# Performance work log

Measured on AMD Instinct MI355X. Metric: run time of the kernel, lower is better.

Reference implementation:

```python
import jax, jax.numpy as jnp
import numpy as np

ALPHA = 1.702  # sigmoid-GLU scale
LIMIT = 7.0    # clamp limit
TOP_K = 2      # num_experts_per_tok


def setup_inputs() -> dict:
    key = jax.random.key(0)
    ks = jax.random.split(key, 4)
    B, S, H, E, I = 2, 1024, 1024, 8, 2048
    return {
        "hidden_states": jax.random.normal(ks[0], (B, S, H), jnp.float32),
        "router_weight": jax.random.normal(ks[1], (E, H), jnp.float32),
        "router_bias": jnp.zeros((E,), jnp.float32),
        "gate_up_proj": jax.random.normal(ks[2], (E, H, 2 * I), jnp.float32) * 0.02,
        "gate_up_bias": jnp.zeros((E, 2 * I), jnp.float32),
        "down_proj": jax.random.normal(ks[3], (E, I, H), jnp.float32) * 0.02,
        "down_bias": jnp.zeros((E, H), jnp.float32),
    }


def reference(hidden_states, router_weight, router_bias, gate_up_proj,
              gate_up_bias, down_proj, down_bias):
    B, S, H = hidden_states.shape
    E, _, two_I = gate_up_proj.shape
    I = two_I // 2

    flat = hidden_states.reshape(B * S, H)  # [T, H]

    # Router: softmax + top-k
    logits = flat @ router_weight.T + router_bias            # [T, E]
    scores = jax.nn.softmax(logits, axis=-1)
    topk_w, topk_idx = jax.lax.top_k(scores, TOP_K)          # [T, K]

    # Dense per-expert gated FFN (einsum 'abmh,ehn->abemn' computes all experts
    # on all tokens; the reshape/permute dance is a mathematical no-op).
    gu = jnp.einsum('th,ehn->ten', flat, gate_up_proj) + gate_up_bias  # [T, E, 2I]
    gate = jnp.minimum(gu[..., :I], LIMIT)
    up = jnp.clip(gu[..., I:], -LIMIT, LIMIT)
    glu = gate * jax.nn.sigmoid(gate * ALPHA)
    act = (up + 1.0) * glu                                   # [T, E, I]

    down = jnp.einsum('tei,eih->teh', act, down_proj) + down_bias  # [T, E, H]

    # Combine: gather each token's top-k expert outputs, weighted sum.
    gathered = jnp.take_along_axis(down, topk_idx[:, :, None], axis=1)  # [T, K, H]
    out = (gathered * topk_w[:, :, None]).sum(axis=1)        # [T, H]
    return out.reshape(B, S, H)
```

## Files before the change

### kernel.cpp

```cpp
#include <hip/hip_runtime.h>
#include <math.h>

#define TT 2048
#define HH 1024
#define EE 8
#define II 2048
#define N1 4096
#define ALPHA 1.702f
#define LIMIT 7.0f

typedef __attribute__((ext_vector_type(8))) short short8;
typedef __attribute__((ext_vector_type(4))) float floatx4;

__device__ __forceinline__ short f2bf(float f) {
  union { float f; unsigned u; } v; v.f = f;
  unsigned r = (v.u + 0x7fffu + ((v.u >> 16) & 1u)) >> 16;
  return (short)r;
}
__device__ __forceinline__ float bf2f(unsigned short s) {
  union { unsigned u; float f; } v; v.u = ((unsigned)s) << 16;
  return v.f;
}

__global__ __launch_bounds__(256) void router_kernel(
    const float* __restrict__ x, const float* __restrict__ rw,
    const float* __restrict__ rb, int* __restrict__ topk_idx,
    float* __restrict__ topk_w) {
  const int t = blockIdx.x;
  const float* xr = x + (size_t)t * HH;
  const int lane = threadIdx.x & 63;
  const int wave = threadIdx.x >> 6;
  float xv[16];
#pragma unroll
  for (int i = 0; i < 16; i++) xv[i] = xr[lane + i * 64];
  __shared__ float logits[EE];
#pragma unroll
  for (int ee = 0; ee < 2; ee++) {
    const int e = wave * 2 + ee;
    const float* wr = rw + (size_t)e * HH;
    float s = 0.f;
#pragma unroll
    for (int i = 0; i < 16; i++) s += xv[i] * wr[lane + i * 64];
#pragma unroll
    for (int off = 32; off > 0; off >>= 1) s += __shfl_down(s, off, 64);
    if (lane == 0) logits[e] = s + rb[e];
  }
  __syncthreads();
  if (threadIdx.x == 0) {
    float l[EE], sc[EE];
    float mx = -3.4e38f;
    for (int i = 0; i < EE; i++) { l[i] = logits[i]; mx = fmaxf(mx, l[i]); }
    float sum = 0.f;
    for (int i = 0; i < EE; i++) { sc[i] = expf(l[i] - mx); sum += sc[i]; }
    const float inv = 1.f / sum;
    int i0 = 0;
    for (int i = 1; i < EE; i++) if (sc[i] > sc[i0]) i0 = i;
    int i1 = (i0 == 0) ? 1 : 0;
    for (int i = 0; i < EE; i++) if (i != i0 && sc[i] > sc[i1]) i1 = i;
    topk_idx[t * 2 + 0] = i0;
    topk_idx[t * 2 + 1] = i1;
    topk_w[t * 2 + 0] = sc[i0] * inv;
    topk_w[t * 2 + 1] = sc[i1] * inv;
  }
}

__global__ void assign_kernel(const int* __restrict__ topk_idx,
                              int* __restrict__ counts, int* __restrict__ rows) {
  const int id = blockIdx.x * blockDim.x + threadIdx.x;
  if (id >= TT * 2) return;
  const int e = topk_idx[id];
  const int slot = atomicAdd(&counts[e], 1);
  rows[e * TT + slot] = id;
}

__global__ __launch_bounds__(256) void gemm_gu(
    const float* __restrict__ x, const float* __restrict__ gup,
    const float* __restrict__ gub, const int* __restrict__ counts,
    const int* __restrict__ rows, unsigned short* __restrict__ gu) {
  const int e = blockIdx.z, mtile = blockIdx.y, ntile = blockIdx.x;
  const int count = counts[e];
  if (mtile * 128 >= count) return;
  const int* rl = rows + e * TT + mtile * 128;
  __shared__ short As[128][40];
  __shared__ short Bs[128][40];
  const int tid = threadIdx.x;
  const int lane = tid & 63, wave = tid >> 6;
  const int wm = (wave & 1) << 6, wn = (wave >> 1) << 6;
  const int quad = lane >> 4, r16 = lane & 15;

  const int arow = tid >> 2, akoct = tid & 3;
  const int cr0 = (mtile * 128 + arow < count) ? arow : (count - 1 - mtile * 128);
  const int cr1 = (mtile * 128 + arow + 64 < count) ? arow + 64 : (count - 1 - mtile * 128);
  const float* a0 = x + (size_t)(rl[cr0] >> 1) * HH;
  const float* a1 = x + (size_t)(rl[cr1] >> 1) * HH;

  const int bn = tid & 127, bk = tid >> 7;
  const float* bb = gup + (size_t)e * HH * N1 + ntile * 128 + bn;

  floatx4 acc[4][4] = {};

  for (int k0 = 0; k0 < HH; k0 += 32) {
    __syncthreads();
    {
      const float4* p = (const float4*)(a0 + k0 + akoct * 8);
      float4 v0 = p[0], v1 = p[1];
      short8 s;
      s[0]=f2bf(v0.x); s[1]=f2bf(v0.y); s[2]=f2bf(v0.z); s[3]=f2bf(v0.w);
      s[4]=f2bf(v1.x); s[5]=f2bf(v1.y); s[6]=f2bf(v1.z); s[7]=f2bf(v1.w);
      *(short8*)&As[arow][akoct * 8] = s;
      p = (const float4*)(a1 + k0 + akoct * 8);
      v0 = p[0]; v1 = p[1];
      s[0]=f2bf(v0.x); s[1]=f2bf(v0.y); s[2]=f2bf(v0.z); s[3]=f2bf(v0.w);
      s[4]=f2bf(v1.x); s[5]=f2bf(v1.y); s[6]=f2bf(v1.z); s[7]=f2bf(v1.w);
      *(short8*)&As[arow + 64][akoct * 8] = s;
    }
    {
      const float* p = bb + (size_t)(k0 + bk * 8) * N1;
      short8 s;
#pragma unroll
      for (int j = 0; j < 8; j++) s[j] = f2bf(p[(size_t)j * N1]);
      *(short8*)&Bs[bn][bk * 8] = s;
      p = bb + (size_t)(k0 + (bk + 2) * 8) * N1;
#pragma unroll
      for (int j = 0; j < 8; j++) s[j] = f2bf(p[(size_t)j * N1]);
      *(short8*)&Bs[bn][(bk + 2) * 8] = s;
    }
    __syncthreads();
    short8 af[4], bf_[4];
#pragma unroll
    for (int i = 0; i < 4; i++)
      af[i] = *(const short8*)&As[wm + i * 16 + r16][quad * 8];
#pragma unroll
    for (int j = 0; j < 4; j++)
      bf_[j] = *(const short8*)&Bs[wn + j * 16 + r16][quad * 8];
#pragma unroll
    for (int i = 0; i < 4; i++)
#pragma unroll
      for (int j = 0; j < 4; j++)
        acc[i][j] = __builtin_amdgcn_mfma_f32_16x16x32_bf16(af[i], bf_[j], acc[i][j], 0, 0, 0);
  }
#pragma unroll
  for (int i = 0; i < 4; i++) {
#pragma unroll
    for (int reg = 0; reg < 4; reg++) {
      const int rrow = wm + i * 16 + quad * 4 + reg;
      if (mtile * 128 + rrow < count) {
        const int ent = rl[rrow];
        unsigned short* orow = gu + (size_t)ent * N1 + ntile * 128;
#pragma unroll
        for (int j = 0; j < 4; j++) {
          const int c = wn + j * 16 + r16;
          const float v = acc[i][j][reg] + gub[e * N1 + ntile * 128 + c];
          orow[c] = (unsigned short)f2bf(v);
        }
      }
    }
  }
}

__global__ void act_kernel(const unsigned short* __restrict__ gu,
                           unsigned short* __restrict__ act) {
  const int id = blockIdx.x * blockDim.x + threadIdx.x;
  if (id >= TT * 2 * II) return;
  const int r = id >> 11;
  const int i = id & (II - 1);
  float g = bf2f(gu[(size_t)r * N1 + i]);
  float u = bf2f(gu[(size_t)r * N1 + II + i]);
  g = fminf(g, LIMIT);
  u = fminf(fmaxf(u, -LIMIT), LIMIT);
  const float glu = g / (1.f + expf(-g * ALPHA));
  act[(size_t)r * II + i] = (unsigned short)f2bf((u + 1.f) * glu);
}

__global__ __launch_bounds__(256) void gemm_down(
    const unsigned short* __restrict__ act, const float* __restrict__ dp,
    const float* __restrict__ db, const int* __restrict__ counts,
    const int* __restrict__ rows, float* __restrict__ dout) {
  const int e = blockIdx.z, mtile = blockIdx.y, ntile = blockIdx.x;
  const int count = counts[e];
  if (mtile * 128 >= count) return;
  const int* rl = rows + e * TT + mtile * 128;
  __shared__ short As[128][40];
  __shared__ short Bs[128][40];
  const int tid = threadIdx.x;
  const int lane = tid & 63, wave = tid >> 6;
  const int wm = (wave & 1) << 6, wn = (wave >> 1) << 6;
  const int quad = lane >> 4, r16 = lane & 15;

  const int arow = tid >> 2, akoct = tid & 3;
  const int cr0 = (mtile * 128 + arow < count) ? arow : (count - 1 - mtile * 128);
  const int cr1 = (mtile * 128 + arow + 64 < count) ? arow + 64 : (count - 1 - mtile * 128);
  const unsigned short* a0 = act + (size_t)rl[cr0] * II;
  const unsigned short* a1 = act + (size_t)rl[cr1] * II;

  const int bn = tid & 127, bk = tid >> 7;
  const float* bb = dp + (size_t)e * II * HH + ntile * 128 + bn;

  floatx4 acc[4][4] = {};

  for (int k0 = 0; k0 < II; k0 += 32) {
    __syncthreads();
    {
      *(short8*)&As[arow][akoct * 8] = *(const short8*)(a0 + k0 + akoct * 8);
      *(short8*)&As[arow + 64][akoct * 8] = *(const short8*)(a1 + k0 + akoct * 8);
    }
    {
      const float* p = bb + (size_t)(k0 + bk * 8) * HH;
      short8 s;
#pragma unroll
      for (int j = 0; j < 8; j++) s[j] = f2bf(p[(size_t)j * HH]);
      *(short8*)&Bs[bn][bk * 8] = s;
      p = bb + (size_t)(k0 + (bk + 2) * 8) * HH;
#pragma unroll
      for (int j = 0; j < 8; j++) s[j] = f2bf(p[(size_t)j * HH]);
      *(short8*)&Bs[bn][(bk + 2) * 8] = s;
    }
    __syncthreads();
    short8 af[4], bf_[4];
#pragma unroll
    for (int i = 0; i < 4; i++)
      af[i] = *(const short8*)&As[wm + i * 16 + r16][quad * 8];
#pragma unroll
    for (int j = 0; j < 4; j++)
      bf_[j] = *(const short8*)&Bs[wn + j * 16 + r16][quad * 8];
#pragma unroll
    for (int i = 0; i < 4; i++)
#pragma unroll
      for (int j = 0; j < 4; j++)
        acc[i][j] = __builtin_amdgcn_mfma_f32_16x16x32_bf16(af[i], bf_[j], acc[i][j], 0, 0, 0);
  }
#pragma unroll
  for (int i = 0; i < 4; i++) {
#pragma unroll
    for (int reg = 0; reg < 4; reg++) {
      const int rrow = wm + i * 16 + quad * 4 + reg;
      if (mtile * 128 + rrow < count) {
        const int ent = rl[rrow];
        float* orow = dout + (size_t)ent * HH + ntile * 128;
#pragma unroll
        for (int j = 0; j < 4; j++) {
          const int c = wn + j * 16 + r16;
          orow[c] = acc[i][j][reg] + db[e * HH + ntile * 128 + c];
        }
      }
    }
  }
}

__global__ void combine_kernel(const float* __restrict__ dout,
                               const float* __restrict__ tw,
                               float* __restrict__ out) {
  const int id = blockIdx.x * blockDim.x + threadIdx.x;
  const int t = id >> 8;
  const int h = (id & 255) * 4;
  const float w0 = tw[t * 2], w1 = tw[t * 2 + 1];
  const float4 a = *(const float4*)(dout + (size_t)(2 * t) * HH + h);
  const float4 b = *(const float4*)(dout + (size_t)(2 * t + 1) * HH + h);
  float4 o;
  o.x = w0 * a.x + w1 * b.x;
  o.y = w0 * a.y + w1 * b.y;
  o.z = w0 * a.z + w1 * b.z;
  o.w = w0 * a.w + w1 * b.w;
  *(float4*)(out + (size_t)t * HH + h) = o;
}

extern "C" void kernel_launch(void* const* d_in, const int* in_sizes, int n_in,
                              void* d_out, int out_size, void* d_ws, size_t ws_size,
                              hipStream_t stream) {
  const float* x   = (const float*)d_in[0];
  const float* rw  = (const float*)d_in[1];
  const float* rb  = (const float*)d_in[2];
  const float* gup = (const float*)d_in[3];
  const float* gub = (const float*)d_in[4];
  const float* dp  = (const float*)d_in[5];
  const float* db  = (const float*)d_in[6];
  float* out = (float*)d_out;

  char* ws = (char*)d_ws;
  int*   topk_idx = (int*)(ws + 0);
  float* topk_w   = (float*)(ws + 16384);
  int*   counts   = (int*)(ws + 32768);
  int*   rows     = (int*)(ws + 33024);
  unsigned short* gu  = (unsigned short*)(ws + 131072);
  unsigned short* act = (unsigned short*)(ws + 131072 + 33554432);
  float* dout = (float*)(ws + 131072 + 33554432 + 16777216);

  router_kernel<<<TT, 256, 0, stream>>>(x, rw, rb, topk_idx, topk_w);
  hipMemsetAsync(counts, 0, 64, stream);
  assign_kernel<<<(TT * 2 + 255) / 256, 256, 0, stream>>>(topk_idx, counts, rows);
  gemm_gu<<<dim3(N1 / 128, TT / 128, EE), 256, 0, stream>>>(x, gup, gub, counts, rows, gu);
  act_kernel<<<(TT * 2 * II) / 256, 256, 0, stream>>>(gu, act);
  gemm_down<<<dim3(HH / 128, TT / 128, EE), 256, 0, stream>>>(act, dp, db, counts, rows, dout);
  combine_kernel<<<(TT * HH / 4) / 256, 256, 0, stream>>>(dout, topk_w, out);
}
```

Before: 452.9 us.

## Pre-convert weights to transposed bf16, use global_load_lds, compact schedule, split-K down

Adds pre-pass kernels that convert x to bf16 and transpose/convert both expert weight tensors to K-contiguous bf16 on every call. Both GEMMs can then stage tiles with direct global-to-LDS 16-byte loads into a swizzled layout, replacing the strided scalar fp32 loads and in-loop conversion. A compact schedule of (expert, m-tile) pairs replaces the mostly-empty 3D grid. The down GEMM is split in two along K with atomic accumulation into a zeroed buffer, and its bias moves into combine. The activation kernel is vectorized. The transposes add a full read and write of roughly 200 MB of fp32 weights per call, and the atomics add contention.

```diff
diff --git a/kernel.cpp b/kernel.cpp
--- a/kernel.cpp
+++ b/kernel.cpp
@@ -8,9 +8,15 @@
 #define N1 4096
 #define ALPHA 1.702f
 #define LIMIT 7.0f
+#define MAXSCHED 40
+#define SPLITK 2
 
 typedef __attribute__((ext_vector_type(8))) short short8;
 typedef __attribute__((ext_vector_type(4))) float floatx4;
+
+#define GLL(g, l) __builtin_amdgcn_global_load_lds(                          \
+    (const __attribute__((address_space(1))) void*)(g),                      \
+    (__attribute__((address_space(3))) void*)(l), 16, 0, 0)
 
 __device__ __forceinline__ short f2bf(float f) {
   union { float f; unsigned u; } v; v.f = f;
@@ -20,6 +26,48 @@
 __device__ __forceinline__ float bf2f(unsigned short s) {
   union { unsigned u; float f; } v; v.u = ((unsigned)s) << 16;
   return v.f;
+}
+
+__global__ __launch_bounds__(256) void convert_x(const float* __restrict__ x,
+                                                 unsigned short* __restrict__ xb) {
+  const size_t off = ((size_t)blockIdx.x * blockDim.x + threadIdx.x) * 8;
+  const float4 v0 = *(const float4*)(x + off);
+  const float4 v1 = *(const float4*)(x + off + 4);
+  short8 s;
+  s[0]=f2bf(v0.x); s[1]=f2bf(v0.y); s[2]=f2bf(v0.z); s[3]=f2bf(v0.w);
+  s[4]=f2bf(v1.x); s[5]=f2bf(v1.y); s[6]=f2bf(v1.z); s[7]=f2bf(v1.w);
+  *(short8*)(xb + off) = s;
+}
+
+__global__ __launch_bounds__(256) void transpose_cvt(const float* __restrict__ src,
+                                                     unsigned short* __restrict__ dst,
+                                                     int K, int N) {
+  const int e = blockIdx.z;
+  src += (size_t)e * K * N;
+  dst += (size_t)e * K * N;
+  const int k0 = blockIdx.y * 64, n0 = blockIdx.x * 64;
+  __shared__ unsigned short Ts[64][66];
+  const int tid = threadIdx.x;
+  const int c4 = (tid & 15) * 4;
+  const int r = tid >> 4;
+#pragma unroll
+  for (int i = 0; i < 4; i++) {
+    const int kk = r + i * 16;
+    const float4 v = *(const float4*)(src + (size_t)(k0 + kk) * N + n0 + c4);
+    Ts[kk][c4 + 0] = (unsigned short)f2bf(v.x);
+    Ts[kk][c4 + 1] = (unsigned short)f2bf(v.y);
+    Ts[kk][c4 + 2] = (unsigned short)f2bf(v.z);
+    Ts[kk][c4 + 3] = (unsigned short)f2bf(v.w);
+  }
+  __syncthreads();
+#pragma unroll
+  for (int i = 0; i < 4; i++) {
+    const int nn = r + i * 16;
+    unsigned short o[4];
+#pragma unroll
+    for (int j = 0; j < 4; j++) o[j] = Ts[c4 + j][nn];
+    *(uint2*)(dst + (size_t)(n0 + nn) * K + k0 + c4) = *(const uint2*)o;
+  }
 }
 
 __global__ __launch_bounds__(256) void router_kernel(
@@ -47,11 +95,11 @@
   }
   __syncthreads();
   if (threadIdx.x == 0) {
-    float l[EE], sc[EE];
+    float sc[EE];
     float mx = -3.4e38f;
-    for (int i = 0; i < EE; i++) { l[i] = logits[i]; mx = fmaxf(mx, l[i]); }
+    for (int i = 0; i < EE; i++) mx = fmaxf(mx, logits[i]);
     float sum = 0.f;
-    for (int i = 0; i < EE; i++) { sc[i] = expf(l[i] - mx); sum += sc[i]; }
+    for (int i = 0; i < EE; i++) { sc[i] = expf(logits[i] - mx); sum += sc[i]; }
     const float inv = 1.f / sum;
     int i0 = 0;
     for (int i = 1; i < EE; i++) if (sc[i] > sc[i0]) i0 = i;
@@ -73,194 +121,225 @@
   rows[e * TT + slot] = id;
 }
 
+__global__ void sched_kernel(const int* __restrict__ counts,
+                             int* __restrict__ sched, int* __restrict__ nsched) {
+  if (threadIdx.x == 0) {
+    int n = 0;
+    for (int e = 0; e < EE; e++) {
+      const int mt = (counts[e] + 127) >> 7;
+      for (int m = 0; m < mt; m++) sched[n++] = (e << 8) | m;
+    }
+    nsched[0] = n;
+  }
+}
+
 __global__ __launch_bounds__(256) void gemm_gu(
-    const float* __restrict__ x, const float* __restrict__ gup,
-    const float* __restrict__ gub, const int* __restrict__ counts,
-    const int* __restrict__ rows, unsigned short* __restrict__ gu) {
-  const int e = blockIdx.z, mtile = blockIdx.y, ntile = blockIdx.x;
-  const int count = counts[e];
-  if (mtile * 128 >= count) return;
+    const unsigned short* __restrict__ x_bf,
+    const unsigned short* __restrict__ gup_t,
+    const float* __restrict__ gub,
+    const int* __restrict__ counts, const int* __restrict__ rows,
+    const int* __restrict__ sched, const int* __restrict__ nsched,
+    unsigned short* __restrict__ gu) {
+  const int sid = blockIdx.y;
+  if (sid >= nsched[0]) return;
+  const int sv = sched[sid];
+  const int e = sv >> 8, mtile = sv & 255;
+  const int count = counts[e] - mtile * 128;
+  const int ntile = blockIdx.x;
   const int* rl = rows + e * TT + mtile * 128;
-  __shared__ short As[128][40];
-  __shared__ short Bs[128][40];
+
+  __shared__ short As[128 * 32];
+  __shared__ short Bs[128 * 32];
+
   const int tid = threadIdx.x;
   const int lane = tid & 63, wave = tid >> 6;
+  const int quad = lane >> 4, r16 = lane & 15;
   const int wm = (wave & 1) << 6, wn = (wave >> 1) << 6;
-  const int quad = lane >> 4, r16 = lane & 15;
-
-  const int arow = tid >> 2, akoct = tid & 3;
-  const int cr0 = (mtile * 128 + arow < count) ? arow : (count - 1 - mtile * 128);
-  const int cr1 = (mtile * 128 + arow + 64 < count) ? arow + 64 : (count - 1 - mtile * 128);
-  const float* a0 = x + (size_t)(rl[cr0] >> 1) * HH;
-  const float* a1 = x + (size_t)(rl[cr1] >> 1) * HH;
-
-  const int bn = tid & 127, bk = tid >> 7;
-  const float* bb = gup + (size_t)e * HH * N1 + ntile * 128 + bn;
+
+  const int srow = lane >> 2;
+  const int soct = (lane & 3) ^ (srow & 3);
+  const int lr0 = wave * 32 + srow;
+  const int lr1 = lr0 + 16;
+  const int cr0 = (lr0 < count) ? lr0 : 0;
+  const int cr1 = (lr1 < count) ? lr1 : 0;
+  const unsigned short* aptr0 = x_bf + (size_t)(rl[cr0] >> 1) * HH + soct * 8;
+  const unsigned short* aptr1 = x_bf + (size_t)(rl[cr1] >> 1) * HH + soct * 8;
+  const unsigned short* bptr0 = gup_t + (size_t)e * N1 * HH +
+                                (size_t)(ntile * 128 + lr0) * HH + soct * 8;
+  const unsigned short* bptr1 = bptr0 + (size_t)16 * HH;
+
+  short* lA0 = As + (wave * 32) * 32;
+  short* lA1 = As + (wave * 32 + 16) * 32;
+  short* lB0 = Bs + (wave * 32) * 32;
+  short* lB1 = Bs + (wave * 32 + 16) * 32;
+
+  const int fcol = (quad ^ (r16 & 3)) * 8;
+  const short8* ap[4]; const short8* bp[4];
+#pragma unroll
+  for (int i = 0; i < 4; i++) {
+    ap[i] = (const short8*)&As[(wm + i * 16 + r16) * 32 + fcol];
+    bp[i] = (const short8*)&Bs[(wn + i * 16 + r16) * 32 + fcol];
+  }
 
   floatx4 acc[4][4] = {};
-
   for (int k0 = 0; k0 < HH; k0 += 32) {
     __syncthreads();
-    {
-      const float4* p = (const float4*)(a0 + k0 + akoct * 8);
-      float4 v0 = p[0], v1 = p[1];
-      short8 s;
-      s[0]=f2bf(v0.x); s[1]=f2bf(v0.y); s[2]=f2bf(v0.z); s[3]=f2bf(v0.w);
-      s[4]=f2bf(v1.x); s[5]=f2bf(v1.y); s[6]=f2bf(v1.z); s[7]=f2bf(v1.w);
-      *(short8*)&As[arow][akoct * 8] = s;
-      p = (const float4*)(a1 + k0 + akoct * 8);
-      v0 = p[0]; v1 = p[1];
-      s[0]=f2bf(v0.x); s[1]=f2bf(v0.y); s[2]=f2bf(v0.z); s[3]=f2bf(v0.w);
-      s[4]=f2bf(v1.x); s[5]=f2bf(v1.y); s[6]=f2bf(v1.z); s[7]=f2bf(v1.w);
-      *(short8*)&As[arow + 64][akoct * 8] = s;
-    }
-    {
-      const float* p = bb + (size_t)(k0 + bk * 8) * N1;
-      short8 s;
-#pragma unroll
-      for (int j = 0; j < 8; j++) s[j] = f2bf(p[(size_t)j * N1]);
-      *(short8*)&Bs[bn][bk * 8] = s;
-      p = bb + (size_t)(k0 + (bk + 2) * 8) * N1;
-#pragma unroll
-      for (int j = 0; j < 8; j++) s[j] = f2bf(p[(size_t)j * N1]);
-      *(short8*)&Bs[bn][(bk + 2) * 8] = s;
-    }
+    GLL(aptr0 + k0, lA0);
+    GLL(aptr1 + k0, lA1);
+    GLL(bptr0 + k0, lB0);
+    GLL(bptr1 + k0, lB1);
     __syncthreads();
     short8 af[4], bf_[4];
 #pragma unroll
-    for (int i = 0; i < 4; i++)
-      af[i] = *(const short8*)&As[wm + i * 16 + r16][quad * 8];
-#pragma unroll
-    for (int j = 0; j < 4; j++)
-      bf_[j] = *(const short8*)&Bs[wn + j * 16 + r16][quad * 8];
+    for (int i = 0; i < 4; i++) { af[i] = *ap[i]; bf_[i] = *bp[i]; }
 #pragma unroll
     for (int i = 0; i < 4; i++)
 #pragma unroll
       for (int j = 0; j < 4; j++)
         acc[i][j] = __builtin_amdgcn_mfma_f32_16x16x32_bf16(af[i], bf_[j], acc[i][j], 0, 0, 0);
   }
+
+  const float* bias = gub + (size_t)e * N1 + ntile * 128;
 #pragma unroll
   for (int i = 0; i < 4; i++) {
 #pragma unroll
     for (int reg = 0; reg < 4; reg++) {
       const int rrow = wm + i * 16 + quad * 4 + reg;
-      if (mtile * 128 + rrow < count) {
+      if (rrow < count) {
         const int ent = rl[rrow];
         unsigned short* orow = gu + (size_t)ent * N1 + ntile * 128;
 #pragma unroll
         for (int j = 0; j < 4; j++) {
           const int c = wn + j * 16 + r16;
-          const float v = acc[i][j][reg] + gub[e * N1 + ntile * 128 + c];
-          orow[c] = (unsigned short)f2bf(v);
+          orow[c] = (unsigned short)f2bf(acc[i][j][reg] + bias[c]);
         }
       }
     }
   }
 }
 
-__global__ void act_kernel(const unsigned short* __restrict__ gu,
-                           unsigned short* __restrict__ act) {
+__global__ __launch_bounds__(256) void act_kernel(const unsigned short* __restrict__ gu,
+                                                  unsigned short* __restrict__ act) {
   const int id = blockIdx.x * blockDim.x + threadIdx.x;
-  if (id >= TT * 2 * II) return;
-  const int r = id >> 11;
-  const int i = id & (II - 1);
-  float g = bf2f(gu[(size_t)r * N1 + i]);
-  float u = bf2f(gu[(size_t)r * N1 + II + i]);
-  g = fminf(g, LIMIT);
-  u = fminf(fmaxf(u, -LIMIT), LIMIT);
-  const float glu = g / (1.f + expf(-g * ALPHA));
-  act[(size_t)r * II + i] = (unsigned short)f2bf((u + 1.f) * glu);
+  const int r = id >> 8;
+  const int i8 = (id & 255) * 8;
+  const short8 g8 = *(const short8*)(gu + (size_t)r * N1 + i8);
+  const short8 u8 = *(const short8*)(gu + (size_t)r * N1 + II + i8);
+  short8 o;
+#pragma unroll
+  for (int j = 0; j < 8; j++) {
+    float g = bf2f((unsigned short)g8[j]);
+    float u = bf2f((unsigned short)u8[j]);
+    g = fminf(g, LIMIT);
+    u = fminf(fmaxf(u, -LIMIT), LIMIT);
+    const float glu = g / (1.f + expf(-g * ALPHA));
+    o[j] = f2bf((u + 1.f) * glu);
+  }
+  *(short8*)(act + (size_t)r * II + i8) = o;
 }
 
 __global__ __launch_bounds__(256) void gemm_down(
-    const unsigned short* __restrict__ act, const float* __restrict__ dp,
-    const float* __restrict__ db, const int* __restrict__ counts,
-    const int* __restrict__ rows, float* __restrict__ dout) {
-  const int e = blockIdx.z, mtile = blockIdx.y, ntile = blockIdx.x;
-  const int count = counts[e];
-  if (mtile * 128 >= count) return;
+    const unsigned short* __restrict__ act,
+    const unsigned short* __restrict__ dp_t,
+    const int* __restrict__ counts, const int* __restrict__ rows,
+    const int* __restrict__ sched, const int* __restrict__ nsched,
+    float* __restrict__ dout) {
+  const int sid = blockIdx.y;
+  if (sid >= nsched[0]) return;
+  const int sv = sched[sid];
+  const int e = sv >> 8, mtile = sv & 255;
+  const int count = counts[e] - mtile * 128;
+  const int ntile = blockIdx.x;
+  const int kbase = blockIdx.z * (II / SPLITK);
   const int* rl = rows + e * TT + mtile * 128;
-  __shared__ short As[128][40];
-  __shared__ short Bs[128][40];
+
+  __shared__ short As[128 * 32];
+  __shared__ short Bs[128 * 32];
+
   const int tid = threadIdx.x;
   const int lane = tid & 63, wave = tid >> 6;
+  const int quad = lane >> 4, r16 = lane & 15;
   const int wm = (wave & 1) << 6, wn = (wave >> 1) << 6;
-  const int quad = lane >> 4, r16 = lane & 15;
-
-  const int arow = tid >> 2, akoct = tid & 3;
-  const int cr0 = (mtile * 128 + arow < count) ? arow : (count - 1 - mtile * 128);
-  const int cr1 = (mtile * 128 + arow + 64 < count) ? arow + 64 : (count - 1 - mtile * 128);
-  const unsigned short* a0 = act + (size_t)rl[cr0] * II;
-  const unsigned short* a1 = act + (size_t)rl[cr1] * II;
-
-  const int bn = tid & 127, bk = tid >> 7;
-  const float* bb = dp + (size_t)e * II * HH + ntile * 128 + bn;
+
+  const int srow = lane >> 2;
+  const int soct = (lane & 3) ^ (srow & 3);
+  const int lr0 = wave * 32 + srow;
+  const int lr1 = lr0 + 16;
+  const int cr0 = (lr0 < count) ? lr0 : 0;
+  const int cr1 = (lr1 < count) ? lr1 : 0;
+  const unsigned short* aptr0 = act + (size_t)rl[cr0] * II + soct * 8;
+  const unsigned short* aptr1 = act + (size_t)rl[cr1] * II + soct * 8;
+  const unsigned short* bptr0 = dp_t + (size_t)e * HH * II +
+                                (size_t)(ntile * 128 + lr0) * II + soct * 8;
+  const unsigned short* bptr1 = bptr0 + (size_t)16 * II;
+
+  short* lA0 = As + (wave * 32) * 32;
+  short* lA1 = As + (wave * 32 + 16) * 32;
+  short* lB0 = Bs + (wave * 32) * 32;
+  short* lB1 = Bs + (wave * 32 + 16) * 32;
+
+  const int fcol = (quad ^ (r16 & 3)) * 8;
+  const short8* ap[4]; const short8* bp[4];
+#pragma unroll
+  for (int i = 0; i < 4; i++) {
+    ap[i] = (const short8*)&As[(wm + i * 16 + r16) * 32 + fcol];
+    bp[i] = (const short8*)&Bs[(wn + i * 16 + r16) * 32 + fcol];
+  }
 
   floatx4 acc[4][4] = {};
-
-  for (int k0 = 0; k0 < II; k0 += 32) {
+  for (int k0 = kbase; k0 < kbase + II / SPLITK; k0 += 32) {
     __syncthreads();
-    {
-      *(short8*)&As[arow][akoct * 8] = *(const short8*)(a0 + k0 + akoct * 8);
-      *(short8*)&As[arow + 64][akoct * 8] = *(const short8*)(a1 + k0 + akoct * 8);
-    }
-    {
-      const float* p = bb + (size_t)(k0 + bk * 8) * HH;
-      short8 s;
-#pragma unroll
-      for (int j = 0; j < 8; j++) s[j] = f2bf(p[(size_t)j * HH]);
-      *(short8*)&Bs[bn][bk * 8] = s;
-      p = bb + (size_t)(k0 + (bk + 2) * 8) * HH;
-#pragma unroll
-      for (int j = 0; j < 8; j++) s[j] = f2bf(p[(size_t)j * HH]);
-      *(short8*)&Bs[bn][(bk + 2) * 8] = s;
-    }
+    GLL(aptr0 + k0, lA0);
+    GLL(aptr1 + k0, lA1);
+    GLL(bptr0 + k0, lB0);
+    GLL(bptr1 + k0, lB1);
     __syncthreads();
     short8 af[4], bf_[4];
 #pragma unroll
-    for (int i = 0; i < 4; i++)
-      af[i] = *(const short8*)&As[wm + i * 16 + r16][quad * 8];
-#pragma unroll
-    for (int j = 0; j < 4; j++)
-      bf_[j] = *(const short8*)&Bs[wn + j * 16 + r16][quad * 8];
+    for (int i = 0; i < 4; i++) { af[i] = *ap[i]; bf_[i] = *bp[i]; }
 #pragma unroll
     for (int i = 0; i < 4; i++)
 #pragma unroll
       for (int j = 0; j < 4; j++)
         acc[i][j] = __builtin_amdgcn_mfma_f32_16x16x32_bf16(af[i], bf_[j], acc[i][j], 0, 0, 0);
   }
+
 #pragma unroll
   for (int i = 0; i < 4; i++) {
 #pragma unroll
     for (int reg = 0; reg < 4; reg++) {
       const int rrow = wm + i * 16 + quad * 4 + reg;
-      if (mtile * 128 + rrow < count) {
+      if (rrow < count) {
         const int ent = rl[rrow];
         float* orow = dout + (size_t)ent * HH + ntile * 128;
 #pragma unroll
         for (int j = 0; j < 4; j++) {
           const int c = wn + j * 16 + r16;
-          orow[c] = acc[i][j][reg] + db[e * HH + ntile * 128 + c];
+          atomicAdd(&orow[c], acc[i][j][reg]);
         }
       }
     }
   }
 }
 
-__global__ void combine_kernel(const float* __restrict__ dout,
-                               const float* __restrict__ tw,
-                               float* __restrict__ out) {
+__global__ __launch_bounds__(256) void combine_kernel(
+    const float* __restrict__ dout, const float* __restrict__ tw,
+    const int* __restrict__ tidx, const float* __restrict__ db,
+    float* __restrict__ out) {
   const int id = blockIdx.x * blockDim.x + threadIdx.x;
   const int t = id >> 8;
   const int h = (id & 255) * 4;
   const float w0 = tw[t * 2], w1 = tw[t * 2 + 1];
+  const int e0 = tidx[t * 2], e1 = tidx[t * 2 + 1];
   const float4 a = *(const float4*)(dout + (size_t)(2 * t) * HH + h);
   const float4 b = *(const float4*)(dout + (size_t)(2 * t + 1) * HH + h);
+  const float4 b0 = *(const float4*)(db + (size_t)e0 * HH + h);
+  const float4 b1 = *(const float4*)(db + (size_t)e1 * HH + h);
   float4 o;
-  o.x = w0 * a.x + w1 * b.x;
-  o.y = w0 * a.y + w1 * b.y;
-  o.z = w0 * a.z + w1 * b.z;
-  o.w = w0 * a.w + w1 * b.w;
+  o.x = w0 * (a.x + b0.x) + w1 * (b.x + b1.x);
+  o.y = w0 * (a.y + b0.y) + w1 * (b.y + b1.y);
+  o.z = w0 * (a.z + b0.z) + w1 * (b.z + b1.z);
+  o.w = w0 * (a.w + b0.w) + w1 * (b.w + b1.w);
   *(float4*)(out + (size_t)t * HH + h) = o;
 }
 
@@ -280,16 +359,28 @@
   int*   topk_idx = (int*)(ws + 0);
   float* topk_w   = (float*)(ws + 16384);
   int*   counts   = (int*)(ws + 32768);
-  int*   rows     = (int*)(ws + 33024);
-  unsigned short* gu  = (unsigned short*)(ws + 131072);
-  unsigned short* act = (unsigned short*)(ws + 131072 + 33554432);
-  float* dout = (float*)(ws + 131072 + 33554432 + 16777216);
-
+  int*   nsched   = (int*)(ws + 33024);
+  int*   sched    = (int*)(ws + 33280);
+  int*   rows     = (int*)(ws + 36864);
+  unsigned short* x_bf  = (unsigned short*)(ws + (1u << 20));
+  unsigned short* gup_t = (unsigned short*)(ws + 8388608);
+  unsigned short* act   = (unsigned short*)(ws + 8388608);
+  unsigned short* dp_t  = (unsigned short*)(ws + 75497472);
+  unsigned short* gu    = (unsigned short*)(ws + 109051904);
+  float*          dout  = (float*)(ws + 109051904);
+
+  convert_x<<<TT * HH / (256 * 8), 256, 0, stream>>>(x, x_bf);
+  transpose_cvt<<<dim3(N1 / 64, HH / 64, EE), 256, 0, stream>>>(gup, gup_t, HH, N1);
+  transpose_cvt<<<dim3(HH / 64, II / 64, EE), 256, 0, stream>>>(dp, dp_t, II, HH);
   router_kernel<<<TT, 256, 0, stream>>>(x, rw, rb, topk_idx, topk_w);
   hipMemsetAsync(counts, 0, 64, stream);
   assign_kernel<<<(TT * 2 + 255) / 256, 256, 0, stream>>>(topk_idx, counts, rows);
-  gemm_gu<<<dim3(N1 / 128, TT / 128, EE), 256, 0, stream>>>(x, gup, gub, counts, rows, gu);
-  act_kernel<<<(TT * 2 * II) / 256, 256, 0, stream>>>(gu, act);
-  gemm_down<<<dim3(HH / 128, TT / 128, EE), 256, 0, stream>>>(act, dp, db, counts, rows, dout);
-  combine_kernel<<<(TT * HH / 4) / 256, 256, 0, stream>>>(dout, topk_w, out);
-}
+  sched_kernel<<<1, 64, 0, stream>>>(counts, sched, nsched);
+  gemm_gu<<<dim3(N1 / 128, MAXSCHED), 256, 0, stream>>>(
+      x_bf, gup_t, gub, counts, rows, sched, nsched, gu);
+  act_kernel<<<TT * 2 * II / (256 * 8), 256, 0, stream>>>(gu, act);
+  hipMemsetAsync(dout, 0, (size_t)TT * 2 * HH * 4, stream);
+  gemm_down<<<dim3(HH / 128, MAXSCHED, SPLITK), 256, 0, stream>>>(
+      act, dp_t, counts, rows, sched, nsched, dout);
+  combine_kernel<<<(TT * HH / 4) / 256, 256, 0, stream>>>(dout, topk_w, topk_idx, db, out);
+}
```

New measurement: 455.7 us. No clear change (+0.6%).
